# Kernel tuning notes

Measured on AMD Instinct MI355X. Metric: run time of the kernel, lower is better.

The kernel has to match this reference:

```python
import jax, jax.numpy as jnp
import numpy as np

LN_EPS = 1e-5


def setup_inputs() -> dict:
    key = jax.random.key(0)
    k1, k2 = jax.random.split(key)
    n, c, t, v = 64, 256, 128, 25
    inner2 = 512  # 2 * hidden_dim * n_heads
    return {
        "x": jax.random.normal(k1, (n, c, t, v), dtype=jnp.float32),
        "ln_gamma": jnp.ones((c,), dtype=jnp.float32),
        "ln_beta": jnp.zeros((c,), dtype=jnp.float32),
        "W": jax.random.normal(k2, (inner2, c), dtype=jnp.float32),
        "b": jnp.zeros((inner2,), dtype=jnp.float32),
        "n_heads": 8,
    }


def reference(x, ln_gamma, ln_beta, W, b, n_heads):
    n, c, t, v = x.shape
    inner2 = W.shape[0]
    d = inner2 // 2 // n_heads  # per-head dim
    scale = d ** (-0.5)

    # n c t v -> n t v c
    y = jnp.transpose(x, (0, 2, 3, 1))
    # LayerNorm over channel dim
    mu = jnp.mean(y, axis=-1, keepdims=True)
    var = jnp.mean(jnp.square(y - mu), axis=-1, keepdims=True)
    y = (y - mu) * jax.lax.rsqrt(var + LN_EPS) * ln_gamma + ln_beta
    # QK projection: (n, t, v, 2*h*d)
    y = jnp.einsum('ntvc,ec->ntve', y, W) + b
    q, k = jnp.split(y, 2, axis=-1)

    def heads(z):
        # (n, t, v, h*d) -> (n*t, h, v, d)
        z = z.reshape(n * t, v, n_heads, d)
        return jnp.transpose(z, (0, 2, 1, 3))

    q, k = heads(q), heads(k)
    dots = jnp.einsum('bhid,bhjd->bhij', q, k) * scale
    attn = jax.nn.softmax(dots, axis=-1).astype(jnp.float32)
    return attn
```

## Files before the change

### kernel.cpp

```cpp
#include <hip/hip_runtime.h>
#include <math.h>
#include <stdint.h>

typedef _Float16 f16x8 __attribute__((ext_vector_type(8)));
typedef float    f32x4 __attribute__((ext_vector_type(4)));

#define NB    8192
#define V_    25
#define SCALE_ 0.17677669529663687f
#define LOG2E_ 1.4426950408889634f
#define PP    516

__global__ __launch_bounds__(256)
void prep_w(const float* __restrict__ W, _Float16* __restrict__ ws) {
    int tid  = blockIdx.x * 256 + threadIdx.x;
    int lane = tid & 63;
    int idx  = tid >> 6;
    int C    = idx >> 4;
    int T2   = idx & 15;
    int half = C >> 3, ch = C & 7;
    int l15  = lane & 15, q4 = lane >> 4;
    const float* src = W + (size_t)(half*256 + T2*16 + l15) * 256 + ch*32 + q4*8;
    f16x8 hi, lo;
    #pragma unroll
    for (int j = 0; j < 8; ++j) {
        float w = src[j];
        _Float16 hh = (_Float16)w;
        hi[j] = hh;
        lo[j] = (_Float16)(w - (float)hh);
    }
    char* base = (char*)ws + (size_t)idx * 2048 + lane * 16;
    *(f16x8*)base          = hi;
    *(f16x8*)(base + 1024) = lo;
}

struct SMem {
    union {
        float xbuf[256][36];
        struct {
            _Float16 ysh[32][264];
            _Float16 ysl[32][264];
        } g;
        float p[V_][PP];
    } u;
    float s_mu[32];
    float s_rs[32];
};

__global__ __launch_bounds__(256, 3)
void fused_ln_qk_attn(const float* __restrict__ x,
                      const float* __restrict__ gamma,
                      const float* __restrict__ beta,
                      const _Float16* __restrict__ wsp,
                      const float* __restrict__ bias,
                      float* __restrict__ out)
{
    __shared__ SMem sm;

    const int tid  = threadIdx.x;
    const int lane = tid & 63;
    const int wv   = tid >> 6;
    const int l15  = lane & 15;
    const int q4   = lane >> 4;
    const int nt   = blockIdx.x;
    const int n    = nt >> 7;
    const int t    = nt & 127;
    const int base = n * 819200 + t * 25;

    float xv[32];
    {
        const float* xr = x + base + tid * 3200;
        #pragma unroll
        for (int v = 0; v < V_; ++v) xv[v] = xr[v];
        #pragma unroll
        for (int v = V_; v < 32; ++v) xv[v] = 0.0f;
        #pragma unroll
        for (int i = 0; i < 8; ++i) {
            float4 f;
            f.x = xv[i*4+0]; f.y = xv[i*4+1]; f.z = xv[i*4+2]; f.w = xv[i*4+3];
            *(float4*)&sm.u.xbuf[tid][i*4] = f;
        }
    }
    __syncthreads();

    {
        const int v = tid >> 3;
        const int j = tid & 7;
        float s1 = 0.0f, s2 = 0.0f;
        #pragma unroll 4
        for (int m = 0; m < 32; ++m) {
            float val = sm.u.xbuf[j + 8*m][v];
            s1 += val; s2 += val * val;
        }
        s1 += __shfl_xor(s1, 1); s2 += __shfl_xor(s2, 1);
        s1 += __shfl_xor(s1, 2); s2 += __shfl_xor(s2, 2);
        s1 += __shfl_xor(s1, 4); s2 += __shfl_xor(s2, 4);
        if (j == 0) {
            if (v < V_) {
                float mu  = s1 * (1.0f/256.0f);
                float var = s2 * (1.0f/256.0f) - mu * mu;
                sm.s_mu[v] = mu;
                sm.s_rs[v] = rsqrtf(var + 1e-5f);
            } else { sm.s_mu[v] = 0.0f; sm.s_rs[v] = 0.0f; }
        }
    }
    __syncthreads();

    {
        const float g  = gamma[tid];
        const float be = beta[tid];
        #pragma unroll
        for (int v = 0; v < V_; ++v) {
            float val = (xv[v] - sm.s_mu[v]) * sm.s_rs[v] * g + be;
            _Float16 h = (_Float16)val;
            sm.u.g.ysh[v][tid] = h;
            sm.u.g.ysl[v][tid] = (_Float16)(val - (float)h);
        }
    }
    __syncthreads();

    float bv[2][4];
    #pragma unroll
    for (int h = 0; h < 2; ++h)
        #pragma unroll
        for (int j = 0; j < 4; ++j)
            bv[h][j] = bias[h*256 + (wv*4 + j)*16 + l15];

    f32x4 acc[2][2][4];
    #pragma unroll
    for (int h = 0; h < 2; ++h)
        #pragma unroll
        for (int m = 0; m < 2; ++m)
            #pragma unroll
            for (int j = 0; j < 4; ++j)
                acc[h][m][j] = (f32x4){0.f, 0.f, 0.f, 0.f};

    const char* bbase = (const char*)wsp + (size_t)lane * 16 + (size_t)(wv*4) * 2048;

    for (int ch = 0; ch < 8; ++ch) {
        const int kb = ch*32 + q4*8;
        f16x8 Ah0 = *(const f16x8*)&sm.u.g.ysh[l15][kb];
        f16x8 Ah1 = *(const f16x8*)&sm.u.g.ysh[16 + l15][kb];
        f16x8 Al0 = *(const f16x8*)&sm.u.g.ysl[l15][kb];
        f16x8 Al1 = *(const f16x8*)&sm.u.g.ysl[16 + l15][kb];
        #pragma unroll
        for (int half = 0; half < 2; ++half) {
            const char* cb = bbase + (size_t)(half*8 + ch) * 16 * 2048;
            #pragma unroll
            for (int j = 0; j < 4; ++j) {
                const char* pj = cb + (size_t)j * 2048;
                f16x8 Bh = *(const f16x8*)pj;
                f16x8 Bl = *(const f16x8*)(pj + 1024);
                acc[half][0][j] = __builtin_amdgcn_mfma_f32_16x16x32_f16(Ah0, Bh, acc[half][0][j], 0, 0, 0);
                acc[half][0][j] = __builtin_amdgcn_mfma_f32_16x16x32_f16(Al0, Bh, acc[half][0][j], 0, 0, 0);
                acc[half][0][j] = __builtin_amdgcn_mfma_f32_16x16x32_f16(Ah0, Bl, acc[half][0][j], 0, 0, 0);
                acc[half][1][j] = __builtin_amdgcn_mfma_f32_16x16x32_f16(Ah1, Bh, acc[half][1][j], 0, 0, 0);
                acc[half][1][j] = __builtin_amdgcn_mfma_f32_16x16x32_f16(Al1, Bh, acc[half][1][j], 0, 0, 0);
                acc[half][1][j] = __builtin_amdgcn_mfma_f32_16x16x32_f16(Ah1, Bl, acc[half][1][j], 0, 0, 0);
            }
        }
    }
    __syncthreads();

    #pragma unroll
    for (int half = 0; half < 2; ++half)
        #pragma unroll
        for (int j = 0; j < 4; ++j) {
            int e   = half*256 + (wv*4 + j)*16 + l15;
            int col = (e & ~31) | (((e & 31) + 4*(e >> 5)) & 31);
            #pragma unroll
            for (int mt = 0; mt < 2; ++mt)
                #pragma unroll
                for (int r = 0; r < 4; ++r) {
                    int v = mt*16 + q4*4 + r;
                    if (v < V_) sm.u.p[v][col] = acc[half][mt][j][r] + bv[half][j];
                }
        }
    __syncthreads();

    if (tid < 8 * V_) {
        const int h = tid / V_;
        const int i = tid - h * V_;

        float qv[32];
        #pragma unroll
        for (int dq = 0; dq < 8; ++dq) {
            int c = 32*h + ((4*dq + 4*h) & 31);
            float4 f = *(const float4*)&sm.u.p[i][c];
            qv[dq*4+0] = f.x; qv[dq*4+1] = f.y; qv[dq*4+2] = f.z; qv[dq*4+3] = f.w;
        }

        float s[25];
        float mx = -3.0e38f;
        #pragma unroll
        for (int j = 0; j < V_; ++j) {
            float dot = 0.0f;
            #pragma unroll
            for (int dq = 0; dq < 8; ++dq) {
                int c = 256 + 32*h + ((4*dq + 4*h) & 31);
                float4 f = *(const float4*)&sm.u.p[j][c];
                dot += qv[dq*4+0]*f.x + qv[dq*4+1]*f.y
                     + qv[dq*4+2]*f.z + qv[dq*4+3]*f.w;
            }
            s[j] = dot * SCALE_;
            mx = fmaxf(mx, s[j]);
        }
        float sum = 0.0f;
        #pragma unroll
        for (int j = 0; j < V_; ++j) {
            s[j] = exp2f((s[j] - mx) * LOG2E_);
            sum += s[j];
        }
        const float r = 1.0f / sum;
        float* op = out + (size_t)nt * 5000 + h * 625 + i * 25;
        #pragma unroll
        for (int j = 0; j < V_; ++j) op[j] = s[j] * r;
    }
}

extern "C" void kernel_launch(void* const* d_in, const int* in_sizes, int n_in,
                              void* d_out, int out_size, void* d_ws, size_t ws_size,
                              hipStream_t stream) {
    const float* x     = (const float*)d_in[0];
    const float* gamma = (const float*)d_in[1];
    const float* beta  = (const float*)d_in[2];
    const float* W     = (const float*)d_in[3];
    const float* b     = (const float*)d_in[4];
    _Float16* wsp = (_Float16*)d_ws;
    float* out = (float*)d_out;

    prep_w<<<dim3(64), dim3(256), 0, stream>>>(W, wsp);
    fused_ln_qk_attn<<<dim3(NB), dim3(256), 0, stream>>>(x, gamma, beta, wsp, b, out);
}
```

Baseline: 648.0 us.

## Compute per-head QK^T attention scores with split-fp16 MFMA inside each wave

Replaces the scalar per-thread dot-product attention stage, which used only 200 of 256 threads and read a large fp32 shared buffer, with a per-wave MFMA computation. Each wave writes its own two heads' Q/K projections as hi/lo fp16 pairs into a private shared slab. It then forms the 25x25 score tiles with three compensated MFMAs and does the softmax across lanes with shuffles. This removes a block-wide barrier and most of the scalar FMA work. In exchange it adds padded 32x32 tiles, fp16-split precision error, and output stores scattered across lanes.

```diff
diff --git a/kernel.cpp b/kernel.cpp
--- a/kernel.cpp
+++ b/kernel.cpp
@@ -7,9 +7,7 @@
 
 #define NB    8192
 #define V_    25
-#define SCALE_ 0.17677669529663687f
-#define LOG2E_ 1.4426950408889634f
-#define PP    516
+#define KS_   0.25505003938643f
 
 __global__ __launch_bounds__(256)
 void prep_w(const float* __restrict__ W, _Float16* __restrict__ ws) {
@@ -34,14 +32,14 @@
     *(f16x8*)(base + 1024) = lo;
 }
 
-struct SMem {
+struct __align__(16) SMem {
     union {
         float xbuf[256][36];
         struct {
             _Float16 ysh[32][264];
             _Float16 ysl[32][264];
         } g;
-        float p[V_][PP];
+        _Float16 qk[4][2][32][72];
     } u;
     float s_mu[32];
     float s_rs[32];
@@ -163,58 +161,90 @@
     __syncthreads();
 
     #pragma unroll
-    for (int half = 0; half < 2; ++half)
-        #pragma unroll
-        for (int j = 0; j < 4; ++j) {
-            int e   = half*256 + (wv*4 + j)*16 + l15;
-            int col = (e & ~31) | (((e & 31) + 4*(e >> 5)) & 31);
-            #pragma unroll
-            for (int mt = 0; mt < 2; ++mt)
+    for (int hh = 0; hh < 2; ++hh) {
+        _Float16 (*qh)[72] = sm.u.qk[wv][0];
+        _Float16 (*ql)[72] = sm.u.qk[wv][1];
+
+        #pragma unroll
+        for (int half = 0; half < 2; ++half)
+            #pragma unroll
+            for (int jj = 0; jj < 2; ++jj) {
+                const int  j   = 2*hh + jj;
+                const float bb = bv[half][j];
+                const int  col = half*32 + jj*16 + l15;
+                #pragma unroll
+                for (int mt = 0; mt < 2; ++mt)
+                    #pragma unroll
+                    for (int r = 0; r < 4; ++r) {
+                        const int row = mt*16 + q4*4 + r;
+                        float val  = acc[half][mt][j][r] + bb;
+                        _Float16 h = (_Float16)val;
+                        qh[row][col] = h;
+                        ql[row][col] = (_Float16)(val - (float)h);
+                    }
+            }
+
+        f16x8 Kh[2], Kl[2], Qh[2], Ql[2];
+        #pragma unroll
+        for (int tt = 0; tt < 2; ++tt) {
+            const int rr = tt*16 + l15;
+            Kh[tt] = *(const f16x8*)&qh[rr][32 + q4*8];
+            Kl[tt] = *(const f16x8*)&ql[rr][32 + q4*8];
+            Qh[tt] = *(const f16x8*)&qh[rr][q4*8];
+            Ql[tt] = *(const f16x8*)&ql[rr][q4*8];
+        }
+
+        f32x4 D[2][2];
+        #pragma unroll
+        for (int jt = 0; jt < 2; ++jt)
+            #pragma unroll
+            for (int it = 0; it < 2; ++it) {
+                f32x4 d = (f32x4){0.f, 0.f, 0.f, 0.f};
+                d = __builtin_amdgcn_mfma_f32_16x16x32_f16(Kh[jt], Qh[it], d, 0, 0, 0);
+                d = __builtin_amdgcn_mfma_f32_16x16x32_f16(Kl[jt], Qh[it], d, 0, 0, 0);
+                d = __builtin_amdgcn_mfma_f32_16x16x32_f16(Kh[jt], Ql[it], d, 0, 0, 0);
+                D[jt][it] = d;
+            }
+
+        float* op = out + (size_t)nt * 5000 + (wv*2 + hh) * 625;
+        #pragma unroll
+        for (int it = 0; it < 2; ++it) {
+            const int i = it*16 + l15;
+            float pv[2][4];
+            float mx = -3.0e38f;
+            #pragma unroll
+            for (int jt = 0; jt < 2; ++jt)
                 #pragma unroll
                 for (int r = 0; r < 4; ++r) {
-                    int v = mt*16 + q4*4 + r;
-                    if (v < V_) sm.u.p[v][col] = acc[half][mt][j][r] + bv[half][j];
+                    const int j = jt*16 + q4*4 + r;
+                    float v = (j < V_) ? D[jt][it][r] : -3.0e38f;
+                    pv[jt][r] = v;
+                    mx = fmaxf(mx, v);
                 }
-        }
-    __syncthreads();
-
-    if (tid < 8 * V_) {
-        const int h = tid / V_;
-        const int i = tid - h * V_;
-
-        float qv[32];
-        #pragma unroll
-        for (int dq = 0; dq < 8; ++dq) {
-            int c = 32*h + ((4*dq + 4*h) & 31);
-            float4 f = *(const float4*)&sm.u.p[i][c];
-            qv[dq*4+0] = f.x; qv[dq*4+1] = f.y; qv[dq*4+2] = f.z; qv[dq*4+3] = f.w;
-        }
-
-        float s[25];
-        float mx = -3.0e38f;
-        #pragma unroll
-        for (int j = 0; j < V_; ++j) {
-            float dot = 0.0f;
-            #pragma unroll
-            for (int dq = 0; dq < 8; ++dq) {
-                int c = 256 + 32*h + ((4*dq + 4*h) & 31);
-                float4 f = *(const float4*)&sm.u.p[j][c];
-                dot += qv[dq*4+0]*f.x + qv[dq*4+1]*f.y
-                     + qv[dq*4+2]*f.z + qv[dq*4+3]*f.w;
-            }
-            s[j] = dot * SCALE_;
-            mx = fmaxf(mx, s[j]);
-        }
-        float sum = 0.0f;
-        #pragma unroll
-        for (int j = 0; j < V_; ++j) {
-            s[j] = exp2f((s[j] - mx) * LOG2E_);
-            sum += s[j];
-        }
-        const float r = 1.0f / sum;
-        float* op = out + (size_t)nt * 5000 + h * 625 + i * 25;
-        #pragma unroll
-        for (int j = 0; j < V_; ++j) op[j] = s[j] * r;
+            mx = fmaxf(mx, __shfl_xor(mx, 16));
+            mx = fmaxf(mx, __shfl_xor(mx, 32));
+            float sum = 0.0f;
+            #pragma unroll
+            for (int jt = 0; jt < 2; ++jt)
+                #pragma unroll
+                for (int r = 0; r < 4; ++r) {
+                    float e = exp2f((pv[jt][r] - mx) * KS_);
+                    pv[jt][r] = e;
+                    sum += e;
+                }
+            sum += __shfl_xor(sum, 16);
+            sum += __shfl_xor(sum, 32);
+            const float rcp = 1.0f / sum;
+            if (i < V_) {
+                #pragma unroll
+                for (int jt = 0; jt < 2; ++jt)
+                    #pragma unroll
+                    for (int r = 0; r < 4; ++r) {
+                        const int j = jt*16 + q4*4 + r;
+                        if (j < V_) op[i*25 + j] = pv[jt][r] * rcp;
+                    }
+            }
+        }
     }
 }
 
```

Result: faster. 593.0 us (-8.5%).
